# Optimization experiments

Hardware: AMD Instinct MI355X
Metric: run time of the kernel (lower is better)

Reference implementation:

```python
import jax, jax.numpy as jnp
import numpy as np

N, E = 50000, 800000
IN, H, D = 64, 4, 16          # in_feats, num_heads, head_size (IN == H*D -> identity skip)
NT, ET = 2, 2                 # num node / edge types


def setup_inputs() -> dict:
    key = jax.random.key(0)
    ks = jax.random.split(key, 13)
    s = 0.05
    return {
        "x": jax.random.normal(ks[0], (N, IN), jnp.float32),
        # TypedLinear weights: one [in,out] matrix per node type (DGL TypedLinear, no bias)
        "Wk": jax.random.normal(ks[1], (NT, IN, H * D), jnp.float32) * s,
        "Wq": jax.random.normal(ks[2], (NT, IN, H * D), jnp.float32) * s,
        "Wv": jax.random.normal(ks[3], (NT, IN, H * D), jnp.float32) * s,
        "Wa": jax.random.normal(ks[4], (NT, H * D, H * D), jnp.float32) * s,
        # per-head, per-edge-type relation matrices (relation_att / relation_msg)
        "Ratt": jax.random.normal(ks[5], (H, ET, D, D), jnp.float32) * s,
        "Rmsg": jax.random.normal(ks[6], (H, ET, D, D), jnp.float32) * s,
        "pri": jnp.ones((H, ET), jnp.float32),   # relation_pri
        "skip": jnp.ones((NT,), jnp.float32),    # skip gate per node type
        "ntype": jax.random.randint(ks[7], (N,), 0, NT),
        "etype": jax.random.randint(ks[8], (E,), 0, ET),
        "src": jax.random.randint(ks[9], (E,), 0, N),
        "dst": jax.random.randint(ks[10], (E,), 0, N),
    }


def _typed_linear(x, W, types):
    # x:[N,I], W:[T,I,O], types:[N] -> y[n] = x[n] @ W[types[n]]
    # T is tiny (2): compute all types densely, then select per node.
    y_all = jnp.einsum('ni,tio->tno', x, W)
    return y_all[types, jnp.arange(x.shape[0])]


def reference(x, Wk, Wq, Wv, Wa, Ratt, Rmsg, pri, skip, ntype, etype, src, dst):
    n = x.shape[0]
    k = _typed_linear(x, Wk, ntype).reshape(n, H, D)
    q = _typed_linear(x, Wq, ntype).reshape(n, H, D)
    v = _typed_linear(x, Wv, ntype).reshape(n, H, D)
    # relation transforms per edge type, computed once at node level (ET is tiny),
    # then gathered per edge: equivalent to per-edge TypedLinear in DGL's message fn.
    katt = jnp.einsum('nhd,htdf->thnf', k, Ratt)   # [ET,H,N,D]
    vmsg = jnp.einsum('nhd,htdf->thnf', v, Rmsg)   # [ET,H,N,D]
    kw = katt[etype, :, src]                       # [E,H,D]
    m = vmsg[etype, :, src]                        # [E,H,D]
    qd = q[dst]                                    # [E,H,D]
    # attention logits: (K W_att) . Q * relation_pri / sqrt(d)
    a = (kw * qd).sum(-1) * pri[:, etype].T / jnp.sqrt(jnp.float32(D))  # [E,H]
    # edge softmax over incoming edges of each destination node (stable)
    amax = jax.ops.segment_max(a, dst, num_segments=n)                  # [N,H]
    ae = jnp.exp(a - amax[dst])
    asum = jax.ops.segment_sum(ae, dst, num_segments=n)
    attn = ae / asum[dst]                                               # [E,H]
    # scatter-aggregate messages
    h = jax.ops.segment_sum(m * attn[:, :, None], dst, num_segments=n)  # [N,H,D]
    # target-specific output projection (dropout is identity in eval)
    h = _typed_linear(h.reshape(n, H * D), Wa, ntype)                   # [N,H*D]
    # sigmoid-gated skip (in_feats == H*D so identity residual)
    alpha = jax.nn.sigmoid(skip)[ntype][:, None]
    return h * alpha + x * (1.0 - alpha)
```

## Files before the change

### kernel.cpp

```cpp
#include <hip/hip_runtime.h>
#include <math.h>
#include <stdint.h>

#define N_NODES 50000
#define N_EDGES 800000
#define NT_TYPES 2
#define ET_TYPES 2
#define NB_SCAN ((N_NODES + 255) / 256)
#define M_COLS 320
#define M_PER_T (64 * M_COLS)
#define PROJ_GRID ((N_NODES + 63) / 64)
#define EDGE_GRID ((N_EDGES + 255) / 256)
#define AGG_GRID ((N_NODES + 15) / 16)
#define MAXDEG 64
#define LOG2E 1.44269504088896f
#define HSTRIDE 36

typedef __attribute__((ext_vector_type(8))) short short8v;
typedef __attribute__((ext_vector_type(4))) float float4v;

__device__ __forceinline__ unsigned int f32_to_bf16(float f) {
  unsigned int u = __float_as_uint(f);
  return (u + 0x7FFFu + ((u >> 16) & 1u)) >> 16;
}

__device__ __forceinline__ float row16_sum(float p) {
  int r;
  r = __builtin_amdgcn_update_dpp(0, __float_as_int(p), 0x128, 0xf, 0xf, false);
  p += __int_as_float(r);
  r = __builtin_amdgcn_update_dpp(0, __float_as_int(p), 0x124, 0xf, 0xf, false);
  p += __int_as_float(r);
  r = __builtin_amdgcn_update_dpp(0, __float_as_int(p), 0x122, 0xf, 0xf, false);
  p += __int_as_float(r);
  r = __builtin_amdgcn_update_dpp(0, __float_as_int(p), 0x121, 0xf, 0xf, false);
  p += __int_as_float(r);
  return p;
}

__global__ void zero_kernel(int* __restrict__ deg) {
  const int i = blockIdx.x * 256 + threadIdx.x;
  if (i < N_NODES + 2) deg[i] = 0;
}

__global__ void prep_build_kernel(
    const float* __restrict__ Wk, const float* __restrict__ Wq,
    const float* __restrict__ Wv, const float* __restrict__ Wa,
    const float* __restrict__ Ratt, const float* __restrict__ Rmsg,
    const float* __restrict__ pri,
    const int* __restrict__ dst, const int* __restrict__ src,
    const int* __restrict__ etype, const int* __restrict__ ntype,
    const float* __restrict__ x,
    unsigned short* __restrict__ M2b, unsigned short* __restrict__ Wa2b,
    int* __restrict__ deg, int* __restrict__ tcnt,
    int* __restrict__ tlist, unsigned int* __restrict__ xb,
    int* __restrict__ csr) {
  const int e = blockIdx.x * 256 + threadIdx.x;
  if (e < N_EDGES) {
    int d = dst[e];
    int r = atomicAdd(&deg[d], 1);
    __builtin_nontemporal_store((etype[e] * N_NODES + src[e]) << 6,
                                &csr[(d << 6) + r]);
  }
  if (e < N_NODES * 16) {
    float4 xa = reinterpret_cast<const float4*>(x)[e];
    xb[2 * e]     = f32_to_bf16(xa.x) | (f32_to_bf16(xa.y) << 16);
    xb[2 * e + 1] = f32_to_bf16(xa.z) | (f32_to_bf16(xa.w) << 16);
  }
  if (e < NT_TYPES * 4096) {
    int t = e >> 12;
    int rem = e & 4095;
    int col = rem >> 6, k = rem & 63;
    Wa2b[e] = (unsigned short)f32_to_bf16(Wa[(size_t)t * 4096 + k * 64 + col]);
  }
  if (e < NT_TYPES * M_PER_T) {
    int t = e / M_PER_T;
    int rem = e % M_PER_T;
    int col = rem / 64;
    int k = rem % 64;
    float val;
    if (col < 64) {
      val = Wq[(size_t)t * 4096 + k * 64 + col];
    } else {
      int cc = col - 64;
      int et = cc >> 7;
      int r = cc & 127;
      int c = r >> 1;
      int half = r & 1;
      int h = c >> 4, f = c & 15;
      const float* W = half ? Wv : Wk;
      const float* R = half ? Rmsg : Ratt;
      float s = 0.f;
#pragma unroll
      for (int d = 0; d < 16; ++d)
        s = fmaf(W[(size_t)t * 4096 + k * 64 + h * 16 + d],
                 R[(((size_t)h * ET_TYPES + et) * 16 + d) * 16 + f], s);
      if (half == 0) s *= pri[h * ET_TYPES + et] * 0.25f * LOG2E;
      val = s;
    }
    M2b[e] = (unsigned short)f32_to_bf16(val);
  }
  if (blockIdx.x < NB_SCAN) {
    __shared__ int lcnt[NT_TYPES];
    __shared__ int lbase[NT_TYPES];
    if (threadIdx.x < NT_TYPES) lcnt[threadIdx.x] = 0;
    __syncthreads();
    int t = 0, lpos = 0;
    const bool valid = (e < N_NODES);
    if (valid) {
      t = ntype[e];
      lpos = atomicAdd(&lcnt[t], 1);
    }
    __syncthreads();
    if (threadIdx.x < NT_TYPES)
      lbase[threadIdx.x] = atomicAdd(&tcnt[threadIdx.x], lcnt[threadIdx.x]);
    __syncthreads();
    if (valid)
      tlist[t * N_NODES + lbase[t] + lpos] = e;
  }
}

__global__ __launch_bounds__(256) void proj_kernel(
    const unsigned short* __restrict__ xb,
    const unsigned short* __restrict__ M2b,
    const int* __restrict__ tcnt, const int* __restrict__ tlist,
    unsigned short* __restrict__ qb, unsigned int* __restrict__ kvb) {
  const int ty = blockIdx.x & 1;
  const int pb = blockIdx.x >> 1;
  const int wave = threadIdx.x >> 6;
  const int lane = threadIdx.x & 63;
  const int cnt = __builtin_amdgcn_readfirstlane(tcnt[ty]);
  const int base = (pb * 4 + wave) * 16;
  if (base >= cnt) return;

  const int* lst = tlist + ty * N_NODES;
  const int l15 = lane & 15;
  const int lq = lane >> 4;

  const int nidA = lst[min(base + l15, cnt - 1)];
  const short8v A0 = *reinterpret_cast<const short8v*>(
      xb + (size_t)nidA * 64 + lq * 8);
  const short8v A1 = *reinterpret_cast<const short8v*>(
      xb + (size_t)nidA * 64 + 32 + lq * 8);

  const int n0 = lst[min(base + lq * 4 + 0, cnt - 1)];
  const int n1 = lst[min(base + lq * 4 + 1, cnt - 1)];
  const int n2 = lst[min(base + lq * 4 + 2, cnt - 1)];
  const int n3 = lst[min(base + lq * 4 + 3, cnt - 1)];

  const unsigned short* Bb = M2b + (size_t)ty * M_PER_T;

#pragma unroll
  for (int ct = 0; ct < 20; ++ct) {
    const int colb = ct * 16 + l15;
    const short8v B0 = *reinterpret_cast<const short8v*>(
        Bb + (size_t)colb * 64 + lq * 8);
    const short8v B1 = *reinterpret_cast<const short8v*>(
        Bb + (size_t)colb * 64 + 32 + lq * 8);
    float4v C = {0.f, 0.f, 0.f, 0.f};
    C = __builtin_amdgcn_mfma_f32_16x16x32_bf16(A0, B0, C, 0, 0, 0);
    C = __builtin_amdgcn_mfma_f32_16x16x32_bf16(A1, B1, C, 0, 0, 0);

    if (ct < 4) {
      qb[(size_t)n0 * 64 + colb] = (unsigned short)f32_to_bf16(C[0]);
      qb[(size_t)n1 * 64 + colb] = (unsigned short)f32_to_bf16(C[1]);
      qb[(size_t)n2 * 64 + colb] = (unsigned short)f32_to_bf16(C[2]);
      qb[(size_t)n3 * 64 + colb] = (unsigned short)f32_to_bf16(C[3]);
    } else {
      const float p0 = __shfl_xor(C[0], 1, 64);
      const float p1 = __shfl_xor(C[1], 1, 64);
      const float p2 = __shfl_xor(C[2], 1, 64);
      const float p3 = __shfl_xor(C[3], 1, 64);
      if ((lane & 1) == 0) {
        const int cc = colb - 64;
        const int et = cc >> 7;
        const int c = (cc & 127) >> 1;
        const size_t b0 = ((size_t)et * N_NODES) * 64 + c;
        kvb[b0 + (size_t)n0 * 64] = f32_to_bf16(C[0]) | (f32_to_bf16(p0) << 16);
        kvb[b0 + (size_t)n1 * 64] = f32_to_bf16(C[1]) | (f32_to_bf16(p1) << 16);
        kvb[b0 + (size_t)n2 * 64] = f32_to_bf16(C[2]) | (f32_to_bf16(p2) << 16);
        kvb[b0 + (size_t)n3 * 64] = f32_to_bf16(C[3]) | (f32_to_bf16(p3) << 16);
      }
    }
  }
}

__device__ __forceinline__ void edge_update(unsigned int wrd, float qd,
                                            float& srun, float& acc) {
  float kw = __uint_as_float(wrd << 16);
  float mv = __uint_as_float(wrd & 0xFFFF0000u);
  float w = __builtin_amdgcn_exp2f(row16_sum(kw * qd));
  srun += w;
  acc = fmaf(mv, w, acc);
}

__global__ __launch_bounds__(256) void agg_out_kernel(
    const unsigned short* __restrict__ qb, const unsigned int* __restrict__ kvb,
    const int* __restrict__ deg, const int* __restrict__ csr,
    const unsigned short* __restrict__ Wa2b, const float* __restrict__ x,
    const float* __restrict__ skip, const int* __restrict__ tcnt,
    const int* __restrict__ tlist, float* __restrict__ out) {
  __shared__ unsigned int hlds[16 * HSTRIDE];
  const int wave = threadIdx.x >> 6;
  const int lane = threadIdx.x & 63;
  const int ty = blockIdx.y;
  const int cnt = __builtin_amdgcn_readfirstlane(tcnt[ty]);
  const int base = blockIdx.x * 16;
  if (base >= cnt) return;
  const int* lst = tlist + ty * N_NODES;

  for (int half = 0; half < 2; ++half) {
    const int lrowA = wave * 4 + half * 2;
    int nA = __builtin_amdgcn_readfirstlane(lst[min(base + lrowA, cnt - 1)]);
    int nB = __builtin_amdgcn_readfirstlane(lst[min(base + lrowA + 1, cnt - 1)]);
    const float qdA = __uint_as_float((unsigned int)qb[(size_t)nA * 64 + lane] << 16);
    const float qdB = __uint_as_float((unsigned int)qb[(size_t)nB * 64 + lane] << 16);
    const int eA = __builtin_amdgcn_readfirstlane(deg[nA]);
    const int eB = __builtin_amdgcn_readfirstlane(deg[nB]);
    const int* cA = csr + (nA << 6);
    const int* cB = csr + (nB << 6);

    float sA = 0.f, aA = 0.f, sB = 0.f, aB = 0.f;
    const int m = min(eA, eB);
    int j = 0;
    for (; j + 4 <= m; j += 4) {
      int pA0 = __builtin_amdgcn_readfirstlane(cA[j + 0]);
      int pA1 = __builtin_amdgcn_readfirstlane(cA[j + 1]);
      int pA2 = __builtin_amdgcn_readfirstlane(cA[j + 2]);
      int pA3 = __builtin_amdgcn_readfirstlane(cA[j + 3]);
      int pB0 = __builtin_amdgcn_readfirstlane(cB[j + 0]);
      int pB1 = __builtin_amdgcn_readfirstlane(cB[j + 1]);
      int pB2 = __builtin_amdgcn_readfirstlane(cB[j + 2]);
      int pB3 = __builtin_amdgcn_readfirstlane(cB[j + 3]);
      unsigned int wA0 = kvb[(unsigned)pA0 + lane];
      unsigned int wA1 = kvb[(unsigned)pA1 + lane];
      unsigned int wA2 = kvb[(unsigned)pA2 + lane];
      unsigned int wA3 = kvb[(unsigned)pA3 + lane];
      unsigned int wB0 = kvb[(unsigned)pB0 + lane];
      unsigned int wB1 = kvb[(unsigned)pB1 + lane];
      unsigned int wB2 = kvb[(unsigned)pB2 + lane];
      unsigned int wB3 = kvb[(unsigned)pB3 + lane];
      edge_update(wA0, qdA, sA, aA);
      edge_update(wB0, qdB, sB, aB);
      edge_update(wA1, qdA, sA, aA);
      edge_update(wB1, qdB, sB, aB);
      edge_update(wA2, qdA, sA, aA);
      edge_update(wB2, qdB, sB, aB);
      edge_update(wA3, qdA, sA, aA);
      edge_update(wB3, qdB, sB, aB);
    }
    int jA = j;
    for (; jA + 4 <= eA; jA += 4) {
      int p0 = __builtin_amdgcn_readfirstlane(cA[jA + 0]);
      int p1 = __builtin_amdgcn_readfirstlane(cA[jA + 1]);
      int p2 = __builtin_amdgcn_readfirstlane(cA[jA + 2]);
      int p3 = __builtin_amdgcn_readfirstlane(cA[jA + 3]);
      unsigned int w0 = kvb[(unsigned)p0 + lane];
      unsigned int w1 = kvb[(unsigned)p1 + lane];
      unsigned int w2 = kvb[(unsigned)p2 + lane];
      unsigned int w3 = kvb[(unsigned)p3 + lane];
      edge_update(w0, qdA, sA, aA);
      edge_update(w1, qdA, sA, aA);
      edge_update(w2, qdA, sA, aA);
      edge_update(w3, qdA, sA, aA);
    }
    for (; jA < eA; ++jA) {
      int p = __builtin_amdgcn_readfirstlane(cA[jA]);
      edge_update(kvb[(unsigned)p + lane], qdA, sA, aA);
    }
    int jB = j;
    for (; jB + 4 <= eB; jB += 4) {
      int p0 = __builtin_amdgcn_readfirstlane(cB[jB + 0]);
      int p1 = __builtin_amdgcn_readfirstlane(cB[jB + 1]);
      int p2 = __builtin_amdgcn_readfirstlane(cB[jB + 2]);
      int p3 = __builtin_amdgcn_readfirstlane(cB[jB + 3]);
      unsigned int w0 = kvb[(unsigned)p0 + lane];
      unsigned int w1 = kvb[(unsigned)p1 + lane];
      unsigned int w2 = kvb[(unsigned)p2 + lane];
      unsigned int w3 = kvb[(unsigned)p3 + lane];
      edge_update(w0, qdB, sB, aB);
      edge_update(w1, qdB, sB, aB);
      edge_update(w2, qdB, sB, aB);
      edge_update(w3, qdB, sB, aB);
    }
    for (; jB < eB; ++jB) {
      int p = __builtin_amdgcn_readfirstlane(cB[jB]);
      edge_update(kvb[(unsigned)p + lane], qdB, sB, aB);
    }

    float hvA = (sA > 0.f) ? (aA / sA) : 0.f;
    float hvB = (sB > 0.f) ? (aB / sB) : 0.f;
    float prA = __shfl_xor(hvA, 1, 64);
    float prB = __shfl_xor(hvB, 1, 64);
    if ((lane & 1) == 0) {
      hlds[lrowA * HSTRIDE + (lane >> 1)] =
          f32_to_bf16(hvA) | (f32_to_bf16(prA) << 16);
      hlds[(lrowA + 1) * HSTRIDE + (lane >> 1)] =
          f32_to_bf16(hvB) | (f32_to_bf16(prB) << 16);
    }
  }
  __syncthreads();

  const int l15 = lane & 15;
  const int lq = lane >> 4;
  const short8v A0 = *reinterpret_cast<const short8v*>(&hlds[l15 * HSTRIDE + lq * 4]);
  const short8v A1 = *reinterpret_cast<const short8v*>(&hlds[l15 * HSTRIDE + 16 + lq * 4]);

  const int n0 = lst[min(base + lq * 4 + 0, cnt - 1)];
  const int n1 = lst[min(base + lq * 4 + 1, cnt - 1)];
  const int n2 = lst[min(base + lq * 4 + 2, cnt - 1)];
  const int n3 = lst[min(base + lq * 4 + 3, cnt - 1)];

  const float alpha = 1.f / (1.f + __expf(-skip[ty]));
  const float beta = 1.f - alpha;
  const unsigned short* Bb = Wa2b + (size_t)ty * 4096;

  const int colb = wave * 16 + l15;
  const short8v B0 = *reinterpret_cast<const short8v*>(
      Bb + (size_t)colb * 64 + lq * 8);
  const short8v B1 = *reinterpret_cast<const short8v*>(
      Bb + (size_t)colb * 64 + 32 + lq * 8);
  float4v C = {0.f, 0.f, 0.f, 0.f};
  C = __builtin_amdgcn_mfma_f32_16x16x32_bf16(A0, B0, C, 0, 0, 0);
  C = __builtin_amdgcn_mfma_f32_16x16x32_bf16(A1, B1, C, 0, 0, 0);

  const size_t o0 = (size_t)n0 * 64 + colb;
  const size_t o1 = (size_t)n1 * 64 + colb;
  const size_t o2 = (size_t)n2 * 64 + colb;
  const size_t o3 = (size_t)n3 * 64 + colb;
  out[o0] = C[0] * alpha + x[o0] * beta;
  out[o1] = C[1] * alpha + x[o1] * beta;
  out[o2] = C[2] * alpha + x[o2] * beta;
  out[o3] = C[3] * alpha + x[o3] * beta;
}

extern "C" void kernel_launch(void* const* d_in, const int* in_sizes, int n_in,
                              void* d_out, int out_size, void* d_ws, size_t ws_size,
                              hipStream_t stream) {
  const float* x    = (const float*)d_in[0];
  const float* Wk   = (const float*)d_in[1];
  const float* Wq   = (const float*)d_in[2];
  const float* Wv   = (const float*)d_in[3];
  const float* Wa   = (const float*)d_in[4];
  const float* Ratt = (const float*)d_in[5];
  const float* Rmsg = (const float*)d_in[6];
  const float* pri  = (const float*)d_in[7];
  const float* skip = (const float*)d_in[8];
  const int* ntype  = (const int*)d_in[9];
  const int* etype  = (const int*)d_in[10];
  const int* src    = (const int*)d_in[11];
  const int* dst    = (const int*)d_in[12];
  float* out = (float*)d_out;

  unsigned short* qb = (unsigned short*)d_ws;
  unsigned int* kvb = (unsigned int*)(qb + (size_t)N_NODES * 64);
  unsigned short* xb = (unsigned short*)(kvb + (size_t)ET_TYPES * N_NODES * 64);
  int* deg   = (int*)(xb + (size_t)N_NODES * 64);
  int* tcnt  = deg + N_NODES;
  int* tlist = tcnt + 2;
  int* csr   = tlist + 2 * N_NODES;
  unsigned short* M2b = (unsigned short*)
      (((uintptr_t)(csr + (size_t)N_NODES * MAXDEG) + 255) & ~(uintptr_t)255);
  unsigned short* Wa2b = (unsigned short*)
      (((uintptr_t)(M2b + NT_TYPES * M_PER_T) + 255) & ~(uintptr_t)255);

  zero_kernel<<<NB_SCAN, 256, 0, stream>>>(deg);

  prep_build_kernel<<<EDGE_GRID, 256, 0, stream>>>(
      Wk, Wq, Wv, Wa, Ratt, Rmsg, pri, dst, src, etype, ntype, x,
      M2b, Wa2b, deg, tcnt, tlist, (unsigned int*)xb, csr);

  proj_kernel<<<2 * PROJ_GRID, 256, 0, stream>>>(
      xb, M2b, tcnt, tlist, qb, kvb);

  dim3 agrid(AGG_GRID, NT_TYPES);
  agg_out_kernel<<<agrid, 256, 0, stream>>>(
      qb, (const unsigned int*)kvb, deg, csr, Wa2b, x, skip, tcnt, tlist, out);
}
```

Measured before the change: 123.8 us.

## Fuse edge CSR scatter into projection launch and convert x to bf16 inline

Moves the per-edge degree-count and CSR scatter out of the prep kernel into extra blocks of the projection kernel, so the scatter runs alongside the MFMA projection in a single launch. Each scatter thread now handles four edges, with loads batched before the atomics. The projection converts x rows to bf16 in registers, which removes the separate xb staging buffer and its write and read-back. The prep kernel shrinks to weight packing and the node-type lists on a small grid. In exchange, the projection re-reads fp32 x and competes with atomic-heavy scatter blocks for the same CUs.

```diff
diff --git a/kernel.cpp b/kernel.cpp
--- a/kernel.cpp
+++ b/kernel.cpp
@@ -10,7 +10,7 @@
 #define M_COLS 320
 #define M_PER_T (64 * M_COLS)
 #define PROJ_GRID ((N_NODES + 63) / 64)
-#define EDGE_GRID ((N_EDGES + 255) / 256)
+#define SCAT_GRID ((N_EDGES + 1023) / 1024)
 #define AGG_GRID ((N_NODES + 15) / 16)
 #define MAXDEG 64
 #define LOG2E 1.44269504088896f
@@ -42,39 +42,23 @@
   if (i < N_NODES + 2) deg[i] = 0;
 }
 
-__global__ void prep_build_kernel(
+__global__ void prep_kernel(
     const float* __restrict__ Wk, const float* __restrict__ Wq,
     const float* __restrict__ Wv, const float* __restrict__ Wa,
     const float* __restrict__ Ratt, const float* __restrict__ Rmsg,
-    const float* __restrict__ pri,
-    const int* __restrict__ dst, const int* __restrict__ src,
-    const int* __restrict__ etype, const int* __restrict__ ntype,
-    const float* __restrict__ x,
+    const float* __restrict__ pri, const int* __restrict__ ntype,
     unsigned short* __restrict__ M2b, unsigned short* __restrict__ Wa2b,
-    int* __restrict__ deg, int* __restrict__ tcnt,
-    int* __restrict__ tlist, unsigned int* __restrict__ xb,
-    int* __restrict__ csr) {
-  const int e = blockIdx.x * 256 + threadIdx.x;
-  if (e < N_EDGES) {
-    int d = dst[e];
-    int r = atomicAdd(&deg[d], 1);
-    __builtin_nontemporal_store((etype[e] * N_NODES + src[e]) << 6,
-                                &csr[(d << 6) + r]);
-  }
-  if (e < N_NODES * 16) {
-    float4 xa = reinterpret_cast<const float4*>(x)[e];
-    xb[2 * e]     = f32_to_bf16(xa.x) | (f32_to_bf16(xa.y) << 16);
-    xb[2 * e + 1] = f32_to_bf16(xa.z) | (f32_to_bf16(xa.w) << 16);
-  }
-  if (e < NT_TYPES * 4096) {
-    int t = e >> 12;
-    int rem = e & 4095;
+    int* __restrict__ tcnt, int* __restrict__ tlist) {
+  const int idx = blockIdx.x * 256 + threadIdx.x;
+  if (idx < NT_TYPES * 4096) {
+    int t = idx >> 12;
+    int rem = idx & 4095;
     int col = rem >> 6, k = rem & 63;
-    Wa2b[e] = (unsigned short)f32_to_bf16(Wa[(size_t)t * 4096 + k * 64 + col]);
-  }
-  if (e < NT_TYPES * M_PER_T) {
-    int t = e / M_PER_T;
-    int rem = e % M_PER_T;
+    Wa2b[idx] = (unsigned short)f32_to_bf16(Wa[(size_t)t * 4096 + k * 64 + col]);
+  }
+  if (idx < NT_TYPES * M_PER_T) {
+    int t = idx / M_PER_T;
+    int rem = idx % M_PER_T;
     int col = rem / 64;
     int k = rem % 64;
     float val;
@@ -97,17 +81,17 @@
       if (half == 0) s *= pri[h * ET_TYPES + et] * 0.25f * LOG2E;
       val = s;
     }
-    M2b[e] = (unsigned short)f32_to_bf16(val);
-  }
-  if (blockIdx.x < NB_SCAN) {
+    M2b[idx] = (unsigned short)f32_to_bf16(val);
+  }
+  {
     __shared__ int lcnt[NT_TYPES];
     __shared__ int lbase[NT_TYPES];
     if (threadIdx.x < NT_TYPES) lcnt[threadIdx.x] = 0;
     __syncthreads();
     int t = 0, lpos = 0;
-    const bool valid = (e < N_NODES);
+    const bool valid = (idx < N_NODES);
     if (valid) {
-      t = ntype[e];
+      t = ntype[idx];
       lpos = atomicAdd(&lcnt[t], 1);
     }
     __syncthreads();
@@ -115,17 +99,40 @@
       lbase[threadIdx.x] = atomicAdd(&tcnt[threadIdx.x], lcnt[threadIdx.x]);
     __syncthreads();
     if (valid)
-      tlist[t * N_NODES + lbase[t] + lpos] = e;
-  }
-}
-
-__global__ __launch_bounds__(256) void proj_kernel(
-    const unsigned short* __restrict__ xb,
+      tlist[t * N_NODES + lbase[t] + lpos] = idx;
+  }
+}
+
+__global__ __launch_bounds__(256) void projscatter_kernel(
+    const float* __restrict__ x,
     const unsigned short* __restrict__ M2b,
     const int* __restrict__ tcnt, const int* __restrict__ tlist,
-    unsigned short* __restrict__ qb, unsigned int* __restrict__ kvb) {
-  const int ty = blockIdx.x & 1;
-  const int pb = blockIdx.x >> 1;
+    unsigned short* __restrict__ qb, unsigned int* __restrict__ kvb,
+    const int* __restrict__ src, const int* __restrict__ dst,
+    const int* __restrict__ etype, int* __restrict__ deg,
+    int* __restrict__ csr) {
+  const int bid = blockIdx.x;
+  if (bid >= 2 * PROJ_GRID) {
+    const int ebase = (bid - 2 * PROJ_GRID) * 1024 + threadIdx.x;
+    int dsts[4], recs[4];
+#pragma unroll
+    for (int k = 0; k < 4; ++k) {
+      int e = ebase + k * 256;
+      bool v = (e < N_EDGES);
+      dsts[k] = v ? dst[e] : -1;
+      recs[k] = v ? ((etype[e] * N_NODES + src[e]) << 6) : 0;
+    }
+#pragma unroll
+    for (int k = 0; k < 4; ++k) {
+      if (dsts[k] >= 0) {
+        int r = atomicAdd(&deg[dsts[k]], 1);
+        __builtin_nontemporal_store(recs[k], &csr[(dsts[k] << 6) + r]);
+      }
+    }
+    return;
+  }
+  const int ty = bid & 1;
+  const int pb = bid >> 1;
   const int wave = threadIdx.x >> 6;
   const int lane = threadIdx.x & 63;
   const int cnt = __builtin_amdgcn_readfirstlane(tcnt[ty]);
@@ -137,10 +144,22 @@
   const int lq = lane >> 4;
 
   const int nidA = lst[min(base + l15, cnt - 1)];
-  const short8v A0 = *reinterpret_cast<const short8v*>(
-      xb + (size_t)nidA * 64 + lq * 8);
-  const short8v A1 = *reinterpret_cast<const short8v*>(
-      xb + (size_t)nidA * 64 + 32 + lq * 8);
+  const float4* xr = reinterpret_cast<const float4*>(x + (size_t)nidA * 64);
+  const float4 xa0 = xr[lq * 2 + 0];
+  const float4 xa1 = xr[lq * 2 + 1];
+  const float4 xb0 = xr[8 + lq * 2 + 0];
+  const float4 xb1 = xr[8 + lq * 2 + 1];
+  union { short8v v; unsigned int u[4]; } A0u, A1u;
+  A0u.u[0] = f32_to_bf16(xa0.x) | (f32_to_bf16(xa0.y) << 16);
+  A0u.u[1] = f32_to_bf16(xa0.z) | (f32_to_bf16(xa0.w) << 16);
+  A0u.u[2] = f32_to_bf16(xa1.x) | (f32_to_bf16(xa1.y) << 16);
+  A0u.u[3] = f32_to_bf16(xa1.z) | (f32_to_bf16(xa1.w) << 16);
+  A1u.u[0] = f32_to_bf16(xb0.x) | (f32_to_bf16(xb0.y) << 16);
+  A1u.u[1] = f32_to_bf16(xb0.z) | (f32_to_bf16(xb0.w) << 16);
+  A1u.u[2] = f32_to_bf16(xb1.x) | (f32_to_bf16(xb1.y) << 16);
+  A1u.u[3] = f32_to_bf16(xb1.z) | (f32_to_bf16(xb1.w) << 16);
+  const short8v A0 = A0u.v;
+  const short8v A1 = A1u.v;
 
   const int n0 = lst[min(base + lq * 4 + 0, cnt - 1)];
   const int n1 = lst[min(base + lq * 4 + 1, cnt - 1)];
@@ -353,8 +372,7 @@
 
   unsigned short* qb = (unsigned short*)d_ws;
   unsigned int* kvb = (unsigned int*)(qb + (size_t)N_NODES * 64);
-  unsigned short* xb = (unsigned short*)(kvb + (size_t)ET_TYPES * N_NODES * 64);
-  int* deg   = (int*)(xb + (size_t)N_NODES * 64);
+  int* deg   = (int*)(kvb + (size_t)ET_TYPES * N_NODES * 64);
   int* tcnt  = deg + N_NODES;
   int* tlist = tcnt + 2;
   int* csr   = tlist + 2 * N_NODES;
@@ -365,12 +383,11 @@
 
   zero_kernel<<<NB_SCAN, 256, 0, stream>>>(deg);
 
-  prep_build_kernel<<<EDGE_GRID, 256, 0, stream>>>(
-      Wk, Wq, Wv, Wa, Ratt, Rmsg, pri, dst, src, etype, ntype, x,
-      M2b, Wa2b, deg, tcnt, tlist, (unsigned int*)xb, csr);
-
-  proj_kernel<<<2 * PROJ_GRID, 256, 0, stream>>>(
-      xb, M2b, tcnt, tlist, qb, kvb);
+  prep_kernel<<<NB_SCAN, 256, 0, stream>>>(
+      Wk, Wq, Wv, Wa, Ratt, Rmsg, pri, ntype, M2b, Wa2b, tcnt, tlist);
+
+  projscatter_kernel<<<2 * PROJ_GRID + SCAT_GRID, 256, 0, stream>>>(
+      x, M2b, tcnt, tlist, qb, kvb, src, dst, etype, deg, csr);
 
   dim3 agrid(AGG_GRID, NT_TYPES);
   agg_out_kernel<<<agrid, 256, 0, stream>>>(
```

Result: faster. 115.9 us (-6.4%).
